# Kernel tuning notes

Hardware: AMD Instinct MI355X
Metric: run time of the kernel (lower is better)

The kernel has to match this reference:

```python
import jax, jax.numpy as jnp
import numpy as np

B, P, K = 262144, 10, 1   # batch, matrix size, number of passes
GY = 1.0                   # self.gy


def setup_inputs() -> dict:
    key = jax.random.key(0)
    kA, kN = jax.random.split(key)
    A = jax.random.normal(kA, (B, P, P), dtype=jnp.float32)
    # SPD Theta so that inv(Theta) in forward is well-defined
    Theta = jnp.einsum('bik,bjk->bij', A, A) / P + 2.0 * jnp.eye(P, dtype=jnp.float32)
    # deterministic stand-in for the per-column torch.randn(p-1) draws (shared across batch)
    noise = jax.random.normal(kN, (K, P, P - 1), dtype=jnp.float32)
    return {"Theta": Theta, "noise": noise}


def _one_pass(Theta, W, noise_k, gy):
    p = Theta.shape[-1]
    for col in range(p):  # hard sequential column recursion (p=10, static)
        idx = np.concatenate([np.arange(col), np.arange(col + 1, p)])  # indices minus col
        w_22 = W[:, col, col]                     # [B]
        w_12 = W[:, idx, col]                     # [B, p-1]
        W_11 = W[:, idx[:, None], idx[None, :]]   # [B, p-1, p-1]
        # inv(Theta_11) via Schur complement of W
        inv_T11 = W_11 - jnp.einsum('b,bi,bj->bij', 1.0 / w_22, w_12, w_12)
        v = noise_k[col]                          # [p-1], theta_12_next (shared over batch)
        schur = jnp.einsum('i,bij,j->b', v, W_11, v)
        t22n = gy + schur                         # theta_22_next, [B]
        # write updated column/row/diagonal of Theta (equivalent to Theta + Delta)
        Theta = (Theta.at[:, idx, col].set(v[None, :])
                      .at[:, col, idx].set(v[None, :])
                      .at[:, col, col].set(t22n))
        # rank-one update of W (the running inverse)
        w22n = 1.0 / (t22n - jnp.einsum('i,bij,j->b', v, inv_T11, v))
        w12n = -w22n[:, None] * jnp.einsum('bij,j->bi', inv_T11, v)
        W = W.at[:, idx[:, None], idx[None, :]].set(
            inv_T11 + jnp.einsum('b,bi,bj->bij', w22n, w12n, w12n))
        W = (W.at[:, idx, col].set(w12n)
              .at[:, col, idx].set(w12n)
              .at[:, col, col].set(w22n))
    return Theta, W


def reference(Theta, noise):
    # forward: W = inv(Theta).detach(), then K passes of the column recursion
    W = jax.lax.stop_gradient(jnp.linalg.inv(Theta))
    for k in range(noise.shape[0]):
        Theta, W = _one_pass(Theta, W, noise[k], GY)
    return Theta
```

## Files before the change

### kernel.cpp

```cpp
#include <hip/hip_runtime.h>

#define P 10
#define PM 9
#define TRI(a,b) ((a)*((a)+1)/2 + (b))

__device__ __forceinline__ int tri_sym(int a, int b) { return a >= b ? TRI(a, b) : TRI(b, a); }

__global__ __launch_bounds__(256, 1)
void spodnet_kernel(const float* __restrict__ Theta,
                    const float* __restrict__ noise,
                    float* __restrict__ out,
                    int B, int K)
{
    int b = blockIdx.x * blockDim.x + threadIdx.x;
    if (b >= B) return;

    float tin[P * P];
    const float4* tp = reinterpret_cast<const float4*>(Theta + (size_t)b * (P * P));
#pragma unroll
    for (int q = 0; q < (P * P) / 4; q++) {
        float4 t = tp[q];
        tin[4 * q + 0] = t.x; tin[4 * q + 1] = t.y;
        tin[4 * q + 2] = t.z; tin[4 * q + 3] = t.w;
    }
    float Tl[55];
#pragma unroll
    for (int i = 0; i < P; i++)
#pragma unroll
        for (int j = 0; j <= i; j++)
            Tl[TRI(i, j)] = tin[i * P + j];

#pragma unroll
    for (int j = 0; j < P; j++) {
        float s = Tl[TRI(j, j)];
#pragma unroll
        for (int k = 0; k < j; k++) s -= Tl[TRI(j, k)] * Tl[TRI(j, k)];
        float ljj = sqrtf(s);
        float ilj = 1.0f / ljj;
        Tl[TRI(j, j)] = ljj;
#pragma unroll
        for (int i = j + 1; i < P; i++) {
            float s2 = Tl[TRI(i, j)];
#pragma unroll
            for (int k = 0; k < j; k++) s2 -= Tl[TRI(i, k)] * Tl[TRI(j, k)];
            Tl[TRI(i, j)] = s2 * ilj;
        }
    }

    float Li[55];
#pragma unroll
    for (int j = 0; j < P; j++) {
        float idj = 1.0f / Tl[TRI(j, j)];
        Li[TRI(j, j)] = idj;
#pragma unroll
        for (int i = j + 1; i < P; i++) {
            float s = 0.f;
#pragma unroll
            for (int k = j; k < i; k++) s += Tl[TRI(i, k)] * Li[TRI(k, j)];
            Li[TRI(i, j)] = -s / Tl[TRI(i, i)];
        }
    }

    float Wl[55];
#pragma unroll
    for (int i = 0; i < P; i++)
#pragma unroll
        for (int j = 0; j <= i; j++) {
            float s = 0.f;
#pragma unroll
            for (int k = i; k < P; k++) s += Li[TRI(k, i)] * Li[TRI(k, j)];
            Wl[TRI(i, j)] = s;
        }

    float diag[P];
    const float gy = 1.0f;
    for (int k = 0; k < K; k++) {
#pragma unroll
        for (int col = 0; col < P; col++) {
            float v_[PM], w12[PM], y_[PM];
#pragma unroll
            for (int t = 0; t < PM; t++) v_[t] = noise[k * P * PM + col * PM + t];
            float w22 = Wl[TRI(col, col)];
#pragma unroll
            for (int t = 0; t < PM; t++) {
                int it = t < col ? t : t + 1;
                w12[t] = Wl[tri_sym(it, col)];
            }
#pragma unroll
            for (int t = 0; t < PM; t++) {
                int it = t < col ? t : t + 1;
                float s = 0.f;
#pragma unroll
                for (int u = 0; u < PM; u++) {
                    int iu = u < col ? u : u + 1;
                    s += Wl[tri_sym(it, iu)] * v_[u];
                }
                y_[t] = s;
            }
            float d = 0.f, schur = 0.f;
#pragma unroll
            for (int t = 0; t < PM; t++) { d += w12[t] * v_[t]; schur += v_[t] * y_[t]; }
            float t22n = gy + schur;
            diag[col] = t22n;
            float dw = d / w22;
            float u_[PM]; float s1 = 0.f;
#pragma unroll
            for (int t = 0; t < PM; t++) { u_[t] = y_[t] - dw * w12[t]; s1 += v_[t] * u_[t]; }
            float w22n = 1.0f / (t22n - s1);
            float w12n[PM];
#pragma unroll
            for (int t = 0; t < PM; t++) w12n[t] = -w22n * u_[t];
            float a = -1.0f / w22;
#pragma unroll
            for (int t = 0; t < PM; t++) {
                int it = t < col ? t : t + 1;
#pragma unroll
                for (int u2 = 0; u2 <= t; u2++) {
                    int iu = u2 < col ? u2 : u2 + 1;
                    Wl[TRI(it, iu)] += a * w12[t] * w12[u2] + w22n * w12n[t] * w12n[u2];
                }
            }
#pragma unroll
            for (int t = 0; t < PM; t++) {
                int it = t < col ? t : t + 1;
                Wl[tri_sym(it, col)] = w12n[t];
            }
            Wl[TRI(col, col)] = w22n;
        }
    }

    const float* nl = noise + (size_t)(K - 1) * P * PM;
    float4* op = reinterpret_cast<float4*>(out + (size_t)b * (P * P));
#pragma unroll
    for (int q = 0; q < (P * P) / 4; q++) {
        float ov[4];
#pragma unroll
        for (int c = 0; c < 4; c++) {
            int e = 4 * q + c; int i = e / P, j = e % P;
            ov[c] = (i == j) ? diag[i] : nl[(i > j ? i : j) * PM + (i < j ? i : j)];
        }
        float4 o; o.x = ov[0]; o.y = ov[1]; o.z = ov[2]; o.w = ov[3];
        op[q] = o;
    }
}

extern "C" void kernel_launch(void* const* d_in, const int* in_sizes, int n_in,
                              void* d_out, int out_size, void* d_ws, size_t ws_size,
                              hipStream_t stream) {
    const float* Theta = (const float*)d_in[0];
    const float* noise = (const float*)d_in[1];
    float* out = (float*)d_out;
    int B = in_sizes[0] / (P * P);
    int K = in_sizes[1] / (P * PM);
    int threads = 256;
    int blocks = (B + threads - 1) / threads;
    hipLaunchKernelGGL(spodnet_kernel, dim3(blocks), dim3(threads), 0, stream,
                       Theta, noise, out, B, K);
}
```

Baseline: 226.1 us.

## Cut register footprint with in-place Cholesky inverse and raise occupancy

Merges the separate tin, Tl, Li and Wl arrays into one 55-entry packed triangle. The Cholesky factor, its triangular inverse and W = L^-T L^-1 are all computed in place, storing reciprocal diagonals via rsq. Launch bounds move from 1 to 4 blocks per CU so the lower register count can give more waves. Exact divisions become hardware rcp/rsq approximations and the rank-one update hoists per-row products. This aims to reduce VGPR pressure, scratch spills and divide latency, at the cost of slightly lower floating-point accuracy.

```diff
diff --git a/kernel.cpp b/kernel.cpp
--- a/kernel.cpp
+++ b/kernel.cpp
@@ -6,7 +6,7 @@
 
 __device__ __forceinline__ int tri_sym(int a, int b) { return a >= b ? TRI(a, b) : TRI(b, a); }
 
-__global__ __launch_bounds__(256, 1)
+__global__ __launch_bounds__(256, 4)
 void spodnet_kernel(const float* __restrict__ Theta,
                     const float* __restrict__ noise,
                     float* __restrict__ out,
@@ -15,62 +15,62 @@
     int b = blockIdx.x * blockDim.x + threadIdx.x;
     if (b >= B) return;
 
-    float tin[P * P];
+    float Wl[55];
     const float4* tp = reinterpret_cast<const float4*>(Theta + (size_t)b * (P * P));
 #pragma unroll
     for (int q = 0; q < (P * P) / 4; q++) {
         float4 t = tp[q];
-        tin[4 * q + 0] = t.x; tin[4 * q + 1] = t.y;
-        tin[4 * q + 2] = t.z; tin[4 * q + 3] = t.w;
+        float c4[4] = {t.x, t.y, t.z, t.w};
+#pragma unroll
+        for (int c = 0; c < 4; c++) {
+            int e = 4 * q + c;
+            int i = e / P, j = e % P;
+            if (i >= j) Wl[TRI(i, j)] = c4[c];
+        }
     }
-    float Tl[55];
-#pragma unroll
-    for (int i = 0; i < P; i++)
-#pragma unroll
-        for (int j = 0; j <= i; j++)
-            Tl[TRI(i, j)] = tin[i * P + j];
 
 #pragma unroll
     for (int j = 0; j < P; j++) {
-        float s = Tl[TRI(j, j)];
+        float s = Wl[TRI(j, j)];
 #pragma unroll
-        for (int k = 0; k < j; k++) s -= Tl[TRI(j, k)] * Tl[TRI(j, k)];
-        float ljj = sqrtf(s);
-        float ilj = 1.0f / ljj;
-        Tl[TRI(j, j)] = ljj;
+        for (int k = 0; k < j; k++) s -= Wl[TRI(j, k)] * Wl[TRI(j, k)];
+        float ilj = __builtin_amdgcn_rsqf(s);
+        Wl[TRI(j, j)] = ilj;
 #pragma unroll
         for (int i = j + 1; i < P; i++) {
-            float s2 = Tl[TRI(i, j)];
+            float s2 = Wl[TRI(i, j)];
 #pragma unroll
-            for (int k = 0; k < j; k++) s2 -= Tl[TRI(i, k)] * Tl[TRI(j, k)];
-            Tl[TRI(i, j)] = s2 * ilj;
+            for (int k = 0; k < j; k++) s2 -= Wl[TRI(i, k)] * Wl[TRI(j, k)];
+            Wl[TRI(i, j)] = s2 * ilj;
         }
     }
 
-    float Li[55];
 #pragma unroll
-    for (int j = 0; j < P; j++) {
-        float idj = 1.0f / Tl[TRI(j, j)];
-        Li[TRI(j, j)] = idj;
+    for (int i = 0; i < P; i++) {
 #pragma unroll
-        for (int i = j + 1; i < P; i++) {
-            float s = 0.f;
+        for (int j = i + 1; j < P; j++) {
+            float s = Wl[TRI(j, i)] * Wl[TRI(i, i)];
 #pragma unroll
-            for (int k = j; k < i; k++) s += Tl[TRI(i, k)] * Li[TRI(k, j)];
-            Li[TRI(i, j)] = -s / Tl[TRI(i, i)];
+            for (int k = i + 1; k < j; k++) s += Wl[TRI(j, k)] * Wl[TRI(k, i)];
+            Wl[TRI(j, i)] = -s * Wl[TRI(j, j)];
         }
     }
 
-    float Wl[55];
 #pragma unroll
-    for (int i = 0; i < P; i++)
+    for (int j = 0; j < P; j++) {
+        float ajj = Wl[TRI(j, j)];
 #pragma unroll
-        for (int j = 0; j <= i; j++) {
-            float s = 0.f;
+        for (int i = 0; i < j; i++) {
+            float s = ajj * Wl[TRI(j, i)];
 #pragma unroll
-            for (int k = i; k < P; k++) s += Li[TRI(k, i)] * Li[TRI(k, j)];
-            Wl[TRI(i, j)] = s;
+            for (int k = j + 1; k < P; k++) s += Wl[TRI(k, j)] * Wl[TRI(k, i)];
+            Wl[TRI(j, i)] = s;
         }
+        float sd = ajj * ajj;
+#pragma unroll
+        for (int k = j + 1; k < P; k++) sd += Wl[TRI(k, j)] * Wl[TRI(k, j)];
+        Wl[TRI(j, j)] = sd;
+    }
 
     float diag[P];
     const float gy = 1.0f;
@@ -102,28 +102,29 @@
             for (int t = 0; t < PM; t++) { d += w12[t] * v_[t]; schur += v_[t] * y_[t]; }
             float t22n = gy + schur;
             diag[col] = t22n;
-            float dw = d / w22;
-            float u_[PM]; float s1 = 0.f;
+            float dw = d * __builtin_amdgcn_rcpf(w22);
+            float s1 = 0.f;
 #pragma unroll
-            for (int t = 0; t < PM; t++) { u_[t] = y_[t] - dw * w12[t]; s1 += v_[t] * u_[t]; }
-            float w22n = 1.0f / (t22n - s1);
-            float w12n[PM];
+            for (int t = 0; t < PM; t++) { y_[t] = y_[t] - dw * w12[t]; s1 += v_[t] * y_[t]; }
+            float w22n = __builtin_amdgcn_rcpf(t22n - s1);
 #pragma unroll
-            for (int t = 0; t < PM; t++) w12n[t] = -w22n * u_[t];
-            float a = -1.0f / w22;
+            for (int t = 0; t < PM; t++) y_[t] = -w22n * y_[t];
+            float a = -__builtin_amdgcn_rcpf(w22);
 #pragma unroll
             for (int t = 0; t < PM; t++) {
                 int it = t < col ? t : t + 1;
+                float pa = a * w12[t];
+                float pb = w22n * y_[t];
 #pragma unroll
                 for (int u2 = 0; u2 <= t; u2++) {
                     int iu = u2 < col ? u2 : u2 + 1;
-                    Wl[TRI(it, iu)] += a * w12[t] * w12[u2] + w22n * w12n[t] * w12n[u2];
+                    Wl[TRI(it, iu)] += pa * w12[u2] + pb * y_[u2];
                 }
             }
 #pragma unroll
             for (int t = 0; t < PM; t++) {
                 int it = t < col ? t : t + 1;
-                Wl[tri_sym(it, col)] = w12n[t];
+                Wl[tri_sym(it, col)] = y_[t];
             }
             Wl[TRI(col, col)] = w22n;
         }
```

Result: slower. 441.0 us (+95.1%).
